# Kernel tuning notes

Hardware: AMD Instinct MI355X
Metric: run time of the kernel (lower is better)

## Reference

```python
import jax, jax.numpy as jnp
import numpy as np
from math import sqrt

D_MODEL = 1024
N_HEADS = 16
D_T = 256
D_HID = 4 * D_MODEL
EPS = 1e-6


def _rmsnorm(x):
    # RMSNorm without affine: x / sqrt(mean(x^2) + eps)
    return x * jax.lax.rsqrt(jnp.mean(x * x, axis=-1, keepdims=True) + EPS)


def setup_inputs() -> dict:
    key = jax.random.key(0)
    ks = jax.random.split(key, 16)
    s = 0.02  # weight init scale
    inp = {
        "x": jax.random.normal(ks[0], (4, 2048, D_MODEL), dtype=jnp.float32),
        "t": jax.random.normal(ks[1], (4, D_T), dtype=jnp.float32),
        # AdaRMSNorm (attn) : Linear(d_t, d_model, bias=False) weights stored (out, in)
        "attn_gamma_w": jax.random.normal(ks[2], (D_MODEL, D_T), dtype=jnp.float32) * s,
        "attn_beta_w": jax.random.normal(ks[3], (D_MODEL, D_T), dtype=jnp.float32) * s,
        # Attention projections
        "W_q": jax.random.normal(ks[4], (D_MODEL, D_MODEL), dtype=jnp.float32) * s,
        "W_k": jax.random.normal(ks[5], (D_MODEL, D_MODEL), dtype=jnp.float32) * s,
        "W_v": jax.random.normal(ks[6], (D_MODEL, D_MODEL), dtype=jnp.float32) * s,
        "W_o": jax.random.normal(ks[7], (D_MODEL, D_MODEL), dtype=jnp.float32) * s,
        "attn_alpha_w": jax.random.normal(ks[8], (D_MODEL, D_T), dtype=jnp.float32) * s,
        # AdaRMSNorm (ffn)
        "ffn_gamma_w": jax.random.normal(ks[9], (D_MODEL, D_T), dtype=jnp.float32) * s,
        "ffn_beta_w": jax.random.normal(ks[10], (D_MODEL, D_T), dtype=jnp.float32) * s,
        # SwiGLU
        "gate_w": jax.random.normal(ks[11], (D_HID, D_MODEL), dtype=jnp.float32) * s,
        "hidden_w": jax.random.normal(ks[12], (D_HID, D_MODEL), dtype=jnp.float32) * s,
        "out_w": jax.random.normal(ks[13], (D_MODEL, D_HID), dtype=jnp.float32) * s,
        "out_b": jnp.zeros((D_MODEL,), dtype=jnp.float32),
        "ffn_alpha_w": jax.random.normal(ks[14], (D_MODEL, D_T), dtype=jnp.float32) * s,
    }
    return inp


def _ada_rmsnorm(x, t, gamma_w, beta_w):
    gamma = (t @ gamma_w.T)[:, None, :]  # [b, 1, d]
    beta = (t @ beta_w.T)[:, None, :]
    return gamma * _rmsnorm(x) + beta


def _attention(x, W_q, W_k, W_v, W_o):
    b, l, dm = x.shape
    d_head = dm // N_HEADS
    scale = sqrt(N_HEADS / dm)  # == 1/sqrt(d_head)
    def split(y):  # [b, l, dm] -> [b, n, l, d]
        return y.reshape(b, l, N_HEADS, d_head).transpose(0, 2, 1, 3)
    q = split(x @ W_q.T)
    k = split(x @ W_k.T)
    v = split(x @ W_v.T)
    attn = jax.nn.softmax(scale * jnp.einsum("bnqd,bnkd->bnqk", q, k), axis=-1)
    o = jnp.einsum("bnqk,bnkd->bnqd", attn, v)
    o = o.transpose(0, 2, 1, 3).reshape(b, l, dm)
    return o @ W_o.T


def _swiglu(x, gate_w, hidden_w, out_w, out_b):
    return (jax.nn.silu(x @ gate_w.T) * (x @ hidden_w.T)) @ out_w.T + out_b


def reference(x, t, attn_gamma_w, attn_beta_w, W_q, W_k, W_v, W_o, attn_alpha_w,
              ffn_gamma_w, ffn_beta_w, gate_w, hidden_w, out_w, out_b, ffn_alpha_w):
    a_alpha = (t @ attn_alpha_w.T)[:, None, :]
    x = x + a_alpha * _attention(_ada_rmsnorm(x, t, attn_gamma_w, attn_beta_w), W_q, W_k, W_v, W_o)
    f_alpha = (t @ ffn_alpha_w.T)[:, None, :]
    return x + f_alpha * _swiglu(_ada_rmsnorm(x, t, ffn_gamma_w, ffn_beta_w), gate_w, hidden_w, out_w, out_b)
```

## Files before the change

### kernel.cpp

```cpp
#include <hip/hip_runtime.h>
#include <hip/hip_bf16.h>

typedef __attribute__((ext_vector_type(8))) short short8;
typedef __attribute__((ext_vector_type(4))) short short4v;
typedef __attribute__((ext_vector_type(4))) float f32x4;
using bf16 = __hip_bfloat16;

#define BARF()  asm volatile("s_barrier" ::: "memory")
#define LGKM0() asm volatile("s_waitcnt lgkmcnt(0)" ::: "memory")
#define VMC4()  asm volatile("s_waitcnt vmcnt(4)" ::: "memory")
#define VMC0()  asm volatile("s_waitcnt vmcnt(0)" ::: "memory")
#define PRIO1() __builtin_amdgcn_s_setprio(1)
#define PRIO0() __builtin_amdgcn_s_setprio(0)

static __device__ __forceinline__ short bfb(float f) {
  bf16 h = __float2bfloat16(f);
  short r; __builtin_memcpy(&r, &h, 2); return r;
}

static __device__ __forceinline__ void gld_lds16(const bf16* g, bf16* l) {
  __builtin_amdgcn_global_load_lds(
      (const __attribute__((address_space(1))) void*)g,
      (__attribute__((address_space(3))) void*)l, 16, 0, 0);
}

__global__ __launch_bounds__(256) void cvt_all_kernel(
    const float* __restrict__ s0, const float* __restrict__ s1, const float* __restrict__ s2,
    const float* __restrict__ s3, const float* __restrict__ gw, const float* __restrict__ hw,
    const float* __restrict__ ow, bf16* __restrict__ dbase) {
  size_t c = (size_t)blockIdx.x * 256 + threadIdx.x;
  const float* src; size_t se;
  if (c < 524288) {
    int seg = (int)(c >> 17);
    src = (seg == 0) ? s0 : (seg == 1) ? s1 : (seg == 2) ? s2 : s3;
    se = (c - ((size_t)seg << 17)) * 8;
  } else if (c < 1572864) {
    size_t lc = c - 524288;
    size_t row = lc >> 7;
    src = (row & 1) ? hw : gw;
    se = ((row >> 1) << 10) + ((lc & 127) << 3);
  } else { src = ow; se = (c - 1572864) * 8; }
  float4 v0 = *(const float4*)(src + se);
  float4 v1 = *(const float4*)(src + se + 4);
  short8 o;
  o[0] = bfb(v0.x); o[1] = bfb(v0.y); o[2] = bfb(v0.z); o[3] = bfb(v0.w);
  o[4] = bfb(v1.x); o[5] = bfb(v1.y); o[6] = bfb(v1.z); o[7] = bfb(v1.w);
  *(short8*)(dbase + c * 8) = o;
}

__global__ __launch_bounds__(256) void tproj_kernel(const float* __restrict__ t,
    const float* __restrict__ w0, const float* __restrict__ w1, const float* __restrict__ w2,
    const float* __restrict__ w3, const float* __restrict__ w4, const float* __restrict__ w5,
    float* __restrict__ out) {
  int gid = blockIdx.x * 256 + threadIdx.x;
  int s = gid >> 12, rem = gid & 4095;
  int b = rem >> 10, n = rem & 1023;
  const float* w = (s == 0) ? w0 : (s == 1) ? w1 : (s == 2) ? w2 : (s == 3) ? w3 : (s == 4) ? w4 : w5;
  const float4* tv = (const float4*)(t + b * 256);
  const float4* wv = (const float4*)(w + n * 256);
  float acc = 0.f;
  #pragma unroll 8
  for (int j = 0; j < 64; ++j) {
    float4 a = tv[j], c = wv[j];
    acc += a.x * c.x + a.y * c.y + a.z * c.z + a.w * c.w;
  }
  out[gid] = acc;
}

__global__ __launch_bounds__(256) void ada_rms_kernel(const float* __restrict__ x,
    const float* __restrict__ gamma, const float* __restrict__ beta, bf16* __restrict__ out) {
  int row = blockIdx.x;
  int b = row >> 11;
  int tid = threadIdx.x;
  const float* xr = x + (size_t)row * 1024;
  float4 v = *(const float4*)(xr + tid * 4);
  float ss = v.x * v.x + v.y * v.y + v.z * v.z + v.w * v.w;
  #pragma unroll
  for (int m = 1; m < 64; m <<= 1) ss += __shfl_xor(ss, m);
  __shared__ float red[4];
  if ((tid & 63) == 0) red[tid >> 6] = ss;
  __syncthreads();
  float tot = red[0] + red[1] + red[2] + red[3];
  float rinv = rsqrtf(tot * (1.0f / 1024.0f) + 1e-6f);
  const float* g  = gamma + b * 1024 + tid * 4;
  const float* be = beta  + b * 1024 + tid * 4;
  short4v o;
  o[0] = bfb(g[0] * v.x * rinv + be[0]);
  o[1] = bfb(g[1] * v.y * rinv + be[1]);
  o[2] = bfb(g[2] * v.z * rinv + be[2]);
  o[3] = bfb(g[3] * v.w * rinv + be[3]);
  *(short4v*)(out + (size_t)row * 1024 + tid * 4) = o;
}

enum { EPI8_QKV = 0, EPI8_GH = 1 };

template<int EPI>
__global__ __launch_bounds__(512, 2) void gemm8p_kernel(
    const bf16* __restrict__ A, const bf16* __restrict__ B,
    int N, int K,
    bf16* __restrict__ o1, bf16* __restrict__ o2, bf16* __restrict__ o3)
{
  __shared__ __align__(16) bf16 sA[2 * 2 * 128 * 64];
  __shared__ __align__(16) bf16 sB[2 * 2 * 128 * 64];
  const int tid = threadIdx.x;
  const int lane = tid & 63, w = tid >> 6;
  const int wr = w >> 2, wcn = w & 3;
  const int ntn = N >> 8;
  const int trow = (int)(blockIdx.x / ntn) << 8;
  const int tcol = (int)(blockIdx.x % ntn) << 8;
  const int fr = lane & 15, hi = lane >> 4;
  const int rbase = hi << 2;
  const int NITER = K >> 7;
  const int st_row = (w << 4) + (lane >> 3);
  const int st_col = (((lane & 7) ^ ((lane >> 3) & 7)) << 3);
  const bf16* AsH0 = A + (size_t)(trow + st_row) * K + st_col;
  const bf16* AsH1 = AsH0 + (size_t)128 * K;
  const bf16* BsH0 = B + (size_t)(tcol + st_row) * K + st_col;
  const bf16* BsH1 = BsH0 + (size_t)128 * K;
  const size_t K8 = (size_t)K << 3;
  bf16* dA = sA + (w << 10);
  bf16* dB = sB + (w << 10);

  auto stA = [&](int dbuf, int h, int t) {
    const bf16* s = (h ? AsH1 : AsH0) + (t << 6);
    bf16* d = dA + ((dbuf * 2 + h) << 13);
    gld_lds16(s, d);
    gld_lds16(s + K8, d + 512);
  };
  auto stB = [&](int dbuf, int h, int t) {
    const bf16* s = (h ? BsH1 : BsH0) + (t << 6);
    bf16* d = dB + ((dbuf * 2 + h) << 13);
    gld_lds16(s, d);
    gld_lds16(s + K8, d + 512);
  };
  const int colK0 = (hi << 3) ^ ((fr & 7) << 3);
  const int colK1 = (32 + (hi << 3)) ^ ((fr & 7) << 3);
  const bf16* aB[2] = { sA + (wr << 13) + (fr << 6) + colK0,
                        sA + (wr << 13) + (fr << 6) + colK1 };
  const bf16* bB[2] = { sB + ((wcn >> 1) << 13) + ((wcn & 1) << 12) + (fr << 6) + colK0,
                        sB + ((wcn >> 1) << 13) + ((wcn & 1) << 12) + (fr << 6) + colK1 };

  f32x4 acc[8][4] = {};
  short8 a[4][2], b0[2][2], b1[2][2];

  auto RDA = [&](int dbuf, int mh) {
    #pragma unroll
    for (int mq = 0; mq < 4; ++mq)
      #pragma unroll
      for (int kk = 0; kk < 2; ++kk)
        a[mq][kk] = *(const short8*)(aB[kk] + dbuf * 16384 + (mh * 4 + mq) * 1024);
  };
  auto RDB0 = [&](int dbuf, int nh) {
    #pragma unroll
    for (int nq = 0; nq < 2; ++nq)
      #pragma unroll
      for (int kk = 0; kk < 2; ++kk)
        b0[nq][kk] = *(const short8*)(bB[kk] + dbuf * 16384 + (nh * 2 + nq) * 1024);
  };
  auto RDB1 = [&](int dbuf, int nh) {
    #pragma unroll
    for (int nq = 0; nq < 2; ++nq)
      #pragma unroll
      for (int kk = 0; kk < 2; ++kk)
        b1[nq][kk] = *(const short8*)(bB[kk] + dbuf * 16384 + (nh * 2 + nq) * 1024);
  };
  auto QUAD0 = [&](int mh, int nh) {
    #pragma unroll
    for (int kk = 0; kk < 2; ++kk)
      #pragma unroll
      for (int mq = 0; mq < 4; ++mq)
        #pragma unroll
        for (int nq = 0; nq < 2; ++nq)
          acc[mh * 4 + mq][nh * 2 + nq] = __builtin_amdgcn_mfma_f32_16x16x32_bf16(
              a[mq][kk], b0[nq][kk], acc[mh * 4 + mq][nh * 2 + nq], 0, 0, 0);
  };
  auto QUAD1 = [&](int mh, int nh) {
    #pragma unroll
    for (int kk = 0; kk < 2; ++kk)
      #pragma unroll
      for (int mq = 0; mq < 4; ++mq)
        #pragma unroll
        for (int nq = 0; nq < 2; ++nq)
          acc[mh * 4 + mq][nh * 2 + nq] = __builtin_amdgcn_mfma_f32_16x16x32_bf16(
              a[mq][kk], b1[nq][kk], acc[mh * 4 + mq][nh * 2 + nq], 0, 0, 0);
  };

  stB(0, 0, 0); stB(0, 1, 0); stA(0, 0, 0); stA(0, 1, 0);
  stB(1, 0, 1); stB(1, 1, 1);
  VMC4();
  BARF();

  for (int i = 0; i < NITER; ++i) {
    const int t1 = 2 * i + 1, tn0 = 2 * i + 2, tn1 = 2 * i + 3;
    const bool g = (i != NITER - 1);
    RDA(0, 0); RDB0(0, 0);
    stA(1, 0, t1);
    BARF(); LGKM0(); PRIO1(); QUAD0(0, 0); PRIO0(); BARF();
    RDB1(0, 1);
    stA(1, 1, t1);
    BARF(); LGKM0(); PRIO1(); QUAD1(0, 1); PRIO0(); BARF();
    RDA(0, 1);
    if (g) stB(0, 0, tn0);
    BARF(); LGKM0(); PRIO1(); QUAD1(1, 1); PRIO0(); BARF();
    if (g) stB(0, 1, tn0);
    BARF(); LGKM0(); PRIO1(); QUAD0(1, 0); PRIO0();
    if (g) { VMC4(); } else { VMC0(); }
    BARF();
    RDA(1, 0); RDB0(1, 0);
    if (g) stA(0, 0, tn0);
    BARF(); LGKM0(); PRIO1(); QUAD0(0, 0); PRIO0(); BARF();
    RDB1(1, 1);
    if (g) stA(0, 1, tn0);
    BARF(); LGKM0(); PRIO1(); QUAD1(0, 1); PRIO0(); BARF();
    RDA(1, 1);
    if (g) stB(1, 0, tn1);
    BARF(); LGKM0(); PRIO1(); QUAD1(1, 1); PRIO0(); BARF();
    if (g) stB(1, 1, tn1);
    BARF(); LGKM0(); PRIO1(); QUAD0(1, 0); PRIO0();
    if (g) { VMC4(); }
    BARF();
  }

  #pragma unroll
  for (int m = 0; m < 8; ++m)
  #pragma unroll
  for (int n = 0; n < 4; ++n)
  #pragma unroll
  for (int r = 0; r < 4; ++r) {
    int row = trow + (wr << 7) + m * 16 + rbase + r;
    int col = tcol + (wcn << 6) + n * 16 + fr;
    float c = acc[m][n][r];
    if constexpr (EPI == EPI8_QKV) {
      int seg = col >> 10, cc = col & 1023;
      int b = row >> 11, l = row & 2047, h = cc >> 6, dd = cc & 63;
      if (seg == 0) {
        o1[(((size_t)(b * 16 + h) * 2048 + l) << 6) + dd] = __float2bfloat16(c * 0.18033688f);
      } else if (seg == 1) o2[(((size_t)(b * 16 + h) * 2048 + l) << 6) + dd] = __float2bfloat16(c);
      else               o3[(((size_t)(b * 16 + h) * 64 + dd) << 11) + l] = __float2bfloat16(c);
    } else {
      float other = __shfl_xor(c, 1);
      if (!(fr & 1)) {
        float sg = c / (1.f + __expf(-c));
        o1[(size_t)row * 4096 + (col >> 1)] = __float2bfloat16(sg * other);
      }
    }
  }
}

enum { EPI_RESID = 0, EPI_FINAL = 1 };

template<int EPI>
__global__ __launch_bounds__(256) void gemm_bt_kernel(
    const bf16* __restrict__ A, const bf16* __restrict__ B,
    int N, int K,
    float* __restrict__ outF,
    const float* __restrict__ aux1, const float* __restrict__ aux2,
    const float* __restrict__ bias)
{
  __shared__ __align__(16) bf16 As[128][32];
  __shared__ __align__(16) bf16 Bs[128][32];
  const int tid = threadIdx.x;
  const int lane = tid & 63, wid = tid >> 6;
  const int wr = wid >> 1, wc = wid & 1;
  const int ntn = N >> 7;
  const int trow = (int)(blockIdx.x / ntn) << 7;
  const int tcol = (int)(blockIdx.x % ntn) << 7;
  const int fr = lane & 15, fc = (lane >> 4) << 3;
  const int rbase = (lane >> 4) << 2;
  const bf16* gA0 = A + (size_t)(trow + wid * 32 + (lane >> 2)) * K + ((lane & 3) << 3);
  const bf16* gA1 = gA0 + (size_t)16 * K;
  const bf16* gB0 = B + (size_t)(tcol + wid * 32 + (lane >> 2)) * K + ((lane & 3) << 3);
  const bf16* gB1 = gB0 + (size_t)16 * K;
  bf16* lA0 = &As[wid * 32][0];
  bf16* lA1 = &As[wid * 32 + 16][0];
  bf16* lB0 = &Bs[wid * 32][0];
  bf16* lB1 = &Bs[wid * 32 + 16][0];
  f32x4 acc[4][4] = {};
  for (int k0 = 0; k0 < K; k0 += 32) {
    __syncthreads();
    gld_lds16(gA0 + k0, lA0);
    gld_lds16(gA1 + k0, lA1);
    gld_lds16(gB0 + k0, lB0);
    gld_lds16(gB1 + k0, lB1);
    __syncthreads();
    short8 af[4], bfr[4];
    #pragma unroll
    for (int m = 0; m < 4; ++m) af[m] = *(const short8*)&As[wr * 64 + m * 16 + fr][fc];
    #pragma unroll
    for (int n = 0; n < 4; ++n) bfr[n] = *(const short8*)&Bs[wc * 64 + n * 16 + fr][fc];
    #pragma unroll
    for (int m = 0; m < 4; ++m)
      #pragma unroll
      for (int n = 0; n < 4; ++n)
        acc[m][n] = __builtin_amdgcn_mfma_f32_16x16x32_bf16(af[m], bfr[n], acc[m][n], 0, 0, 0);
  }
  #pragma unroll
  for (int m = 0; m < 4; ++m)
  #pragma unroll
  for (int n = 0; n < 4; ++n)
  #pragma unroll
  for (int r = 0; r < 4; ++r) {
    int row = trow + wr * 64 + m * 16 + rbase + r;
    int col = tcol + wc * 64 + n * 16 + fr;
    float c = acc[m][n][r];
    int b = row >> 11;
    size_t idx = (size_t)row * 1024 + col;
    if constexpr (EPI == EPI_RESID) {
      outF[idx] = aux1[idx] + aux2[b * 1024 + col] * c;
    } else {
      outF[idx] = aux1[idx] + aux2[b * 1024 + col] * (c + bias[col]);
    }
  }
}

__global__ __launch_bounds__(256) void attn_kernel(const bf16* __restrict__ q,
    const bf16* __restrict__ k, const bf16* __restrict__ vt, bf16* __restrict__ o) {
  const int id = blockIdx.x;
  const int bh = (id & 7) * 8 + ((id >> 3) >> 4);
  const int qt = (id >> 3) & 15;
  const int b = bh >> 4, h = bh & 15;
  __shared__ __align__(16) bf16 Ks[64][72];
  __shared__ __align__(16) bf16 Vs[64][72];
  __shared__ __align__(16) bf16 Ps[128][72];
  const int tid = threadIdx.x, lane = tid & 63, w = tid >> 6;
  const int fr = lane & 15, hi = lane >> 4;
  const int fc = hi << 3, rbase = hi << 2;
  const bf16* qbase = q + ((size_t)bh * 2048 + qt * 128) * 64;
  const bf16* kbase = k + (size_t)bh * 2048 * 64;
  const bf16* vbase = vt + (size_t)bh * 64 * 2048;
  short8 qf[2][2];
  #pragma unroll
  for (int nq = 0; nq < 2; ++nq)
    #pragma unroll
    for (int ks = 0; ks < 2; ++ks)
      qf[nq][ks] = *(const short8*)(qbase + (size_t)(w * 32 + nq * 16 + fr) * 64 + ks * 32 + fc);
  short8 onesf;
  #pragma unroll
  for (int j = 0; j < 8; ++j) onesf[j] = (short)0x3F80;
  f32x4 accO[4][2] = {};
  f32x4 accD[2] = {};
  const int sr = tid >> 3, sc = (tid & 7) << 3;
  short8 rk0 = *(const short8*)(kbase + (size_t)sr * 64 + sc);
  short8 rk1 = *(const short8*)(kbase + (size_t)(sr + 32) * 64 + sc);
  short8 rv0 = *(const short8*)(vbase + (size_t)sr * 2048 + sc);
  short8 rv1 = *(const short8*)(vbase + (size_t)(sr + 32) * 2048 + sc);
  for (int kt = 0; kt < 2048; kt += 64) {
    __syncthreads();
    *(short8*)&Ks[sr][sc]      = rk0;
    *(short8*)&Ks[sr + 32][sc] = rk1;
    *(short8*)&Vs[sr][sc]      = rv0;
    *(short8*)&Vs[sr + 32][sc] = rv1;
    __syncthreads();
    if (kt + 64 < 2048) {
      rk0 = *(const short8*)(kbase + (size_t)(kt + 64 + sr) * 64 + sc);
      rk1 = *(const short8*)(kbase + (size_t)(kt + 96 + sr) * 64 + sc);
      rv0 = *(const short8*)(vbase + (size_t)sr * 2048 + kt + 64 + sc);
      rv1 = *(const short8*)(vbase + (size_t)(sr + 32) * 2048 + kt + 64 + sc);
    }
    f32x4 s[4][2] = {};
    #pragma unroll
    for (int ks = 0; ks < 2; ++ks) {
      short8 kf[4];
      #pragma unroll
      for (int mk = 0; mk < 4; ++mk) kf[mk] = *(const short8*)&Ks[mk * 16 + fr][ks * 32 + fc];
      #pragma unroll
      for (int mk = 0; mk < 4; ++mk)
        #pragma unroll
        for (int nq = 0; nq < 2; ++nq)
          s[mk][nq] = __builtin_amdgcn_mfma_f32_16x16x32_bf16(kf[mk], qf[nq][ks], s[mk][nq], 0, 0, 0);
    }
    #pragma unroll
    for (int mk = 0; mk < 4; ++mk)
      #pragma unroll
      for (int nq = 0; nq < 2; ++nq) {
        short4v pk;
        pk[0] = bfb(exp2f(s[mk][nq][0]));
        pk[1] = bfb(exp2f(s[mk][nq][1]));
        pk[2] = bfb(exp2f(s[mk][nq][2]));
        pk[3] = bfb(exp2f(s[mk][nq][3]));
        *(short4v*)&Ps[w * 32 + nq * 16 + fr][mk * 16 + rbase] = pk;
      }
    __syncthreads();
    #pragma unroll
    for (int ks2 = 0; ks2 < 2; ++ks2) {
      short8 av[4], bp[2];
      #pragma unroll
      for (int nd = 0; nd < 4; ++nd) av[nd] = *(const short8*)&Vs[nd * 16 + fr][ks2 * 32 + fc];
      #pragma unroll
      for (int nq = 0; nq < 2; ++nq) bp[nq] = *(const short8*)&Ps[w * 32 + nq * 16 + fr][ks2 * 32 + fc];
      #pragma unroll
      for (int nd = 0; nd < 4; ++nd)
        #pragma unroll
        for (int nq = 0; nq < 2; ++nq)
          accO[nd][nq] = __builtin_amdgcn_mfma_f32_16x16x32_bf16(av[nd], bp[nq], accO[nd][nq], 0, 0, 0);
      #pragma unroll
      for (int nq = 0; nq < 2; ++nq)
        accD[nq] = __builtin_amdgcn_mfma_f32_16x16x32_bf16(onesf, bp[nq], accD[nq], 0, 0, 0);
    }
  }
  float rd[2];
  #pragma unroll
  for (int nq = 0; nq < 2; ++nq) rd[nq] = 1.0f / accD[nq][0];
  #pragma unroll
  for (int nd = 0; nd < 4; ++nd)
    #pragma unroll
    for (int nq = 0; nq < 2; ++nq) {
      short4v ov;
      #pragma unroll
      for (int r = 0; r < 4; ++r) ov[r] = bfb(accO[nd][nq][r] * rd[nq]);
      int qrow = qt * 128 + w * 32 + nq * 16 + fr;
      int col = h * 64 + nd * 16 + rbase;
      *(short4v*)&o[((size_t)b * 2048 + qrow) * 1024 + col] = ov;
    }
}

extern "C" void kernel_launch(void* const* d_in, const int* in_sizes, int n_in,
                              void* d_out, int out_size, void* d_ws, size_t ws_size,
                              hipStream_t stream) {
  (void)in_sizes; (void)n_in; (void)out_size; (void)ws_size;
  const float* x   = (const float*)d_in[0];
  const float* t   = (const float*)d_in[1];
  const float* agw = (const float*)d_in[2];
  const float* abw = (const float*)d_in[3];
  const float* wq  = (const float*)d_in[4];
  const float* wk  = (const float*)d_in[5];
  const float* wv  = (const float*)d_in[6];
  const float* wo  = (const float*)d_in[7];
  const float* aaw = (const float*)d_in[8];
  const float* fgw = (const float*)d_in[9];
  const float* fbw = (const float*)d_in[10];
  const float* gw  = (const float*)d_in[11];
  const float* hw  = (const float*)d_in[12];
  const float* ow  = (const float*)d_in[13];
  const float* ob  = (const float*)d_in[14];
  const float* faw = (const float*)d_in[15];
  float* out = (float*)d_out;

  char* p = (char*)d_ws;
  auto alloc = [&](size_t bytes) -> char* {
    char* r = p; p += (bytes + 255) & ~(size_t)255; return r;
  };
  float* tp    = (float*)alloc((size_t)6 * 4096 * 4);
  bf16* wq_b   = (bf16*)alloc((size_t)1024 * 1024 * 2);
  bf16* wk_b   = (bf16*)alloc((size_t)1024 * 1024 * 2);
  bf16* wv_b   = (bf16*)alloc((size_t)1024 * 1024 * 2);
  bf16* wo_b   = (bf16*)alloc((size_t)1024 * 1024 * 2);
  bf16* wgh_b  = (bf16*)alloc((size_t)8192 * 1024 * 2);
  bf16* wout_b = (bf16*)alloc((size_t)1024 * 4096 * 2);
  bf16* xn_b   = (bf16*)alloc((size_t)8192 * 1024 * 2);
  bf16* q_b    = (bf16*)alloc((size_t)8192 * 1024 * 2);
  bf16* k_b    = (bf16*)alloc((size_t)8192 * 1024 * 2);
  bf16* vt_b   = (bf16*)alloc((size_t)8192 * 1024 * 2);
  bf16* ao_b   = (bf16*)alloc((size_t)8192 * 1024 * 2);
  float* xmid  = (float*)alloc((size_t)8192 * 1024 * 4);
  bf16* gh_b   = (bf16*)alloc((size_t)8192 * 4096 * 2);

  cvt_all_kernel<<<8192, 256, 0, stream>>>(wq, wk, wv, wo, gw, hw, ow, wq_b);
  tproj_kernel<<<96, 256, 0, stream>>>(t, agw, abw, aaw, fgw, fbw, faw, tp);
  ada_rms_kernel<<<8192, 256, 0, stream>>>(x, tp + 0 * 4096, tp + 1 * 4096, xn_b);
  gemm8p_kernel<EPI8_QKV><<<384, 512, 0, stream>>>(xn_b, wq_b, 3072, 1024, q_b, k_b, vt_b);
  attn_kernel<<<1024, 256, 0, stream>>>(q_b, k_b, vt_b, ao_b);
  gemm_bt_kernel<EPI_RESID><<<512, 256, 0, stream>>>(ao_b, wo_b, 1024, 1024, xmid, x, tp + 2 * 4096, nullptr);
  ada_rms_kernel<<<8192, 256, 0, stream>>>(xmid, tp + 3 * 4096, tp + 4 * 4096, xn_b);
  gemm8p_kernel<EPI8_GH><<<1024, 512, 0, stream>>>(xn_b, wgh_b, 8192, 1024, gh_b, nullptr, nullptr);
  gemm_bt_kernel<EPI_FINAL><<<512, 256, 0, stream>>>(gh_b, wout_b, 1024, 4096, out, xmid, tp + 5 * 4096, ob);
}
```

Before: 581.2 us.

## Double-buffer K/V in attention, swizzle block order across XCDs, move QKV to smaller GEMM

The attention kernel now double-buffers the K and V tiles in shared memory, which removes one of the two barriers per key tile and lets global loads for tile i+2 overlap compute on tile i. Both GEMM kernels remap blockIdx so that consecutive tiles are spread across the 8 XCDs, aiming for better L2 locality. The QKV projection moves from the 256x256-tile pipelined kernel (384 blocks) to the simpler 128x128-tile kernel (1536 blocks) to get more parallelism, at the cost of a less efficient inner loop. The extra shared memory for double buffering may reduce attention occupancy.

```diff
diff --git a/kernel.cpp b/kernel.cpp
--- a/kernel.cpp
+++ b/kernel.cpp
@@ -92,22 +92,24 @@
   *(short4v*)(out + (size_t)row * 1024 + tid * 4) = o;
 }
 
-enum { EPI8_QKV = 0, EPI8_GH = 1 };
+enum { EPI8_GH = 1 };
 
 template<int EPI>
 __global__ __launch_bounds__(512, 2) void gemm8p_kernel(
     const bf16* __restrict__ A, const bf16* __restrict__ B,
     int N, int K,
-    bf16* __restrict__ o1, bf16* __restrict__ o2, bf16* __restrict__ o3)
+    bf16* __restrict__ o1)
 {
   __shared__ __align__(16) bf16 sA[2 * 2 * 128 * 64];
   __shared__ __align__(16) bf16 sB[2 * 2 * 128 * 64];
   const int tid = threadIdx.x;
   const int lane = tid & 63, w = tid >> 6;
   const int wr = w >> 2, wcn = w & 3;
+  const int cpx = (int)gridDim.x >> 3;
+  const int bid = ((int)blockIdx.x & 7) * cpx + ((int)blockIdx.x >> 3);
   const int ntn = N >> 8;
-  const int trow = (int)(blockIdx.x / ntn) << 8;
-  const int tcol = (int)(blockIdx.x % ntn) << 8;
+  const int trow = (bid / ntn) << 8;
+  const int tcol = (bid % ntn) << 8;
   const int fr = lane & 15, hi = lane >> 4;
   const int rbase = hi << 2;
   const int NITER = K >> 7;
@@ -230,24 +232,15 @@
     int row = trow + (wr << 7) + m * 16 + rbase + r;
     int col = tcol + (wcn << 6) + n * 16 + fr;
     float c = acc[m][n][r];
-    if constexpr (EPI == EPI8_QKV) {
-      int seg = col >> 10, cc = col & 1023;
-      int b = row >> 11, l = row & 2047, h = cc >> 6, dd = cc & 63;
-      if (seg == 0) {
-        o1[(((size_t)(b * 16 + h) * 2048 + l) << 6) + dd] = __float2bfloat16(c * 0.18033688f);
-      } else if (seg == 1) o2[(((size_t)(b * 16 + h) * 2048 + l) << 6) + dd] = __float2bfloat16(c);
-      else               o3[(((size_t)(b * 16 + h) * 64 + dd) << 11) + l] = __float2bfloat16(c);
-    } else {
-      float other = __shfl_xor(c, 1);
-      if (!(fr & 1)) {
-        float sg = c / (1.f + __expf(-c));
-        o1[(size_t)row * 4096 + (col >> 1)] = __float2bfloat16(sg * other);
-      }
-    }
-  }
-}
-
-enum { EPI_RESID = 0, EPI_FINAL = 1 };
+    float other = __shfl_xor(c, 1);
+    if (!(fr & 1)) {
+      float sg = c / (1.f + __expf(-c));
+      o1[(size_t)row * 4096 + (col >> 1)] = __float2bfloat16(sg * other);
+    }
+  }
+}
+
+enum { EPI_RESID = 0, EPI_FINAL = 1, EPI_QKV3 = 2 };
 
 template<int EPI>
 __global__ __launch_bounds__(256) void gemm_bt_kernel(
@@ -255,16 +248,19 @@
     int N, int K,
     float* __restrict__ outF,
     const float* __restrict__ aux1, const float* __restrict__ aux2,
-    const float* __restrict__ bias)
+    const float* __restrict__ bias,
+    bf16* __restrict__ oq, bf16* __restrict__ okk, bf16* __restrict__ ov)
 {
   __shared__ __align__(16) bf16 As[128][32];
   __shared__ __align__(16) bf16 Bs[128][32];
   const int tid = threadIdx.x;
   const int lane = tid & 63, wid = tid >> 6;
   const int wr = wid >> 1, wc = wid & 1;
+  const int cpx = (int)gridDim.x >> 3;
+  const int bid = ((int)blockIdx.x & 7) * cpx + ((int)blockIdx.x >> 3);
   const int ntn = N >> 7;
-  const int trow = (int)(blockIdx.x / ntn) << 7;
-  const int tcol = (int)(blockIdx.x % ntn) << 7;
+  const int trow = (bid / ntn) << 7;
+  const int tcol = (bid % ntn) << 7;
   const int fr = lane & 15, fc = (lane >> 4) << 3;
   const int rbase = (lane >> 4) << 2;
   const bf16* gA0 = A + (size_t)(trow + wid * 32 + (lane >> 2)) * K + ((lane & 3) << 3);
@@ -303,12 +299,20 @@
     int row = trow + wr * 64 + m * 16 + rbase + r;
     int col = tcol + wc * 64 + n * 16 + fr;
     float c = acc[m][n][r];
-    int b = row >> 11;
-    size_t idx = (size_t)row * 1024 + col;
-    if constexpr (EPI == EPI_RESID) {
-      outF[idx] = aux1[idx] + aux2[b * 1024 + col] * c;
+    if constexpr (EPI == EPI_QKV3) {
+      int seg = col >> 10, cc = col & 1023;
+      int bb = row >> 11, l = row & 2047, h2 = cc >> 6, dd = cc & 63;
+      if (seg == 0)      oq[(((size_t)(bb * 16 + h2) * 2048 + l) << 6) + dd] = __float2bfloat16(c * 0.18033688f);
+      else if (seg == 1) okk[(((size_t)(bb * 16 + h2) * 2048 + l) << 6) + dd] = __float2bfloat16(c);
+      else               ov[(((size_t)(bb * 16 + h2) * 64 + dd) << 11) + l] = __float2bfloat16(c);
     } else {
-      outF[idx] = aux1[idx] + aux2[b * 1024 + col] * (c + bias[col]);
+      int b = row >> 11;
+      size_t idx = (size_t)row * 1024 + col;
+      if constexpr (EPI == EPI_RESID) {
+        outF[idx] = aux1[idx] + aux2[b * 1024 + col] * c;
+      } else {
+        outF[idx] = aux1[idx] + aux2[b * 1024 + col] * (c + bias[col]);
+      }
     }
   }
 }
@@ -319,8 +323,8 @@
   const int bh = (id & 7) * 8 + ((id >> 3) >> 4);
   const int qt = (id >> 3) & 15;
   const int b = bh >> 4, h = bh & 15;
-  __shared__ __align__(16) bf16 Ks[64][72];
-  __shared__ __align__(16) bf16 Vs[64][72];
+  __shared__ __align__(16) bf16 Ks[2][64][72];
+  __shared__ __align__(16) bf16 Vs[2][64][72];
   __shared__ __align__(16) bf16 Ps[128][72];
   const int tid = threadIdx.x, lane = tid & 63, w = tid >> 6;
   const int fr = lane & 15, hi = lane >> 4;
@@ -340,29 +344,35 @@
   f32x4 accO[4][2] = {};
   f32x4 accD[2] = {};
   const int sr = tid >> 3, sc = (tid & 7) << 3;
-  short8 rk0 = *(const short8*)(kbase + (size_t)sr * 64 + sc);
-  short8 rk1 = *(const short8*)(kbase + (size_t)(sr + 32) * 64 + sc);
-  short8 rv0 = *(const short8*)(vbase + (size_t)sr * 2048 + sc);
-  short8 rv1 = *(const short8*)(vbase + (size_t)(sr + 32) * 2048 + sc);
+  *(short8*)&Ks[0][sr][sc]      = *(const short8*)(kbase + (size_t)sr * 64 + sc);
+  *(short8*)&Ks[0][sr + 32][sc] = *(const short8*)(kbase + (size_t)(sr + 32) * 64 + sc);
+  *(short8*)&Vs[0][sr][sc]      = *(const short8*)(vbase + (size_t)sr * 2048 + sc);
+  *(short8*)&Vs[0][sr + 32][sc] = *(const short8*)(vbase + (size_t)(sr + 32) * 2048 + sc);
+  short8 rk0 = *(const short8*)(kbase + (size_t)(64 + sr) * 64 + sc);
+  short8 rk1 = *(const short8*)(kbase + (size_t)(96 + sr) * 64 + sc);
+  short8 rv0 = *(const short8*)(vbase + (size_t)sr * 2048 + 64 + sc);
+  short8 rv1 = *(const short8*)(vbase + (size_t)(sr + 32) * 2048 + 64 + sc);
+  __syncthreads();
   for (int kt = 0; kt < 2048; kt += 64) {
-    __syncthreads();
-    *(short8*)&Ks[sr][sc]      = rk0;
-    *(short8*)&Ks[sr + 32][sc] = rk1;
-    *(short8*)&Vs[sr][sc]      = rv0;
-    *(short8*)&Vs[sr + 32][sc] = rv1;
-    __syncthreads();
+    const int cur = (kt >> 6) & 1;
     if (kt + 64 < 2048) {
-      rk0 = *(const short8*)(kbase + (size_t)(kt + 64 + sr) * 64 + sc);
-      rk1 = *(const short8*)(kbase + (size_t)(kt + 96 + sr) * 64 + sc);
-      rv0 = *(const short8*)(vbase + (size_t)sr * 2048 + kt + 64 + sc);
-      rv1 = *(const short8*)(vbase + (size_t)(sr + 32) * 2048 + kt + 64 + sc);
+      *(short8*)&Ks[cur ^ 1][sr][sc]      = rk0;
+      *(short8*)&Ks[cur ^ 1][sr + 32][sc] = rk1;
+      *(short8*)&Vs[cur ^ 1][sr][sc]      = rv0;
+      *(short8*)&Vs[cur ^ 1][sr + 32][sc] = rv1;
+      if (kt + 128 < 2048) {
+        rk0 = *(const short8*)(kbase + (size_t)(kt + 128 + sr) * 64 + sc);
+        rk1 = *(const short8*)(kbase + (size_t)(kt + 160 + sr) * 64 + sc);
+        rv0 = *(const short8*)(vbase + (size_t)sr * 2048 + kt + 128 + sc);
+        rv1 = *(const short8*)(vbase + (size_t)(sr + 32) * 2048 + kt + 128 + sc);
+      }
     }
     f32x4 s[4][2] = {};
     #pragma unroll
     for (int ks = 0; ks < 2; ++ks) {
       short8 kf[4];
       #pragma unroll
-      for (int mk = 0; mk < 4; ++mk) kf[mk] = *(const short8*)&Ks[mk * 16 + fr][ks * 32 + fc];
+      for (int mk = 0; mk < 4; ++mk) kf[mk] = *(const short8*)&Ks[cur][mk * 16 + fr][ks * 32 + fc];
       #pragma unroll
       for (int mk = 0; mk < 4; ++mk)
         #pragma unroll
@@ -380,12 +390,11 @@
         pk[3] = bfb(exp2f(s[mk][nq][3]));
         *(short4v*)&Ps[w * 32 + nq * 16 + fr][mk * 16 + rbase] = pk;
       }
-    __syncthreads();
     #pragma unroll
     for (int ks2 = 0; ks2 < 2; ++ks2) {
       short8 av[4], bp[2];
       #pragma unroll
-      for (int nd = 0; nd < 4; ++nd) av[nd] = *(const short8*)&Vs[nd * 16 + fr][ks2 * 32 + fc];
+      for (int nd = 0; nd < 4; ++nd) av[nd] = *(const short8*)&Vs[cur][nd * 16 + fr][ks2 * 32 + fc];
       #pragma unroll
       for (int nq = 0; nq < 2; ++nq) bp[nq] = *(const short8*)&Ps[w * 32 + nq * 16 + fr][ks2 * 32 + fc];
       #pragma unroll
@@ -397,6 +406,7 @@
       for (int nq = 0; nq < 2; ++nq)
         accD[nq] = __builtin_amdgcn_mfma_f32_16x16x32_bf16(onesf, bp[nq], accD[nq], 0, 0, 0);
     }
+    __syncthreads();
   }
   float rd[2];
   #pragma unroll
@@ -458,10 +468,11 @@
   cvt_all_kernel<<<8192, 256, 0, stream>>>(wq, wk, wv, wo, gw, hw, ow, wq_b);
   tproj_kernel<<<96, 256, 0, stream>>>(t, agw, abw, aaw, fgw, fbw, faw, tp);
   ada_rms_kernel<<<8192, 256, 0, stream>>>(x, tp + 0 * 4096, tp + 1 * 4096, xn_b);
-  gemm8p_kernel<EPI8_QKV><<<384, 512, 0, stream>>>(xn_b, wq_b, 3072, 1024, q_b, k_b, vt_b);
+  gemm_bt_kernel<EPI_QKV3><<<1536, 256, 0, stream>>>(xn_b, wq_b, 3072, 1024,
+      nullptr, nullptr, nullptr, nullptr, q_b, k_b, vt_b);
   attn_kernel<<<1024, 256, 0, stream>>>(q_b, k_b, vt_b, ao_b);
-  gemm_bt_kernel<EPI_RESID><<<512, 256, 0, stream>>>(ao_b, wo_b, 1024, 1024, xmid, x, tp + 2 * 4096, nullptr);
+  gemm_bt_kernel<EPI_RESID><<<512, 256, 0, stream>>>(ao_b, wo_b, 1024, 1024, xmid, x, tp + 2 * 4096, nullptr, nullptr, nullptr, nullptr);
   ada_rms_kernel<<<8192, 256, 0, stream>>>(xmid, tp + 3 * 4096, tp + 4 * 4096, xn_b);
-  gemm8p_kernel<EPI8_GH><<<1024, 512, 0, stream>>>(xn_b, wgh_b, 8192, 1024, gh_b, nullptr, nullptr);
-  gemm_bt_kernel<EPI_FINAL><<<512, 256, 0, stream>>>(gh_b, wout_b, 1024, 4096, out, xmid, tp + 5 * 4096, ob);
-}
+  gemm8p_kernel<EPI8_GH><<<1024, 512, 0, stream>>>(xn_b, wgh_b, 8192, 1024, gh_b);
+  gemm_bt_kernel<EPI_FINAL><<<512, 256, 0, stream>>>(gh_b, wout_b, 1024, 4096, out, xmid, tp + 5 * 4096, ob, nullptr, nullptr, nullptr);
+}
```

Result: no change. 584.3 us (+0.5%).
